# Kernel tuning notes

Measured on AMD Instinct MI355X. Metric: run time of the kernel, lower is better.

The kernel has to match this reference:

```python
import jax, jax.numpy as jnp
from jax import lax
import numpy as np

I, H, B, S = 512, 1024, 64, 512


def setup_inputs() -> dict:
    key = jax.random.key(0)
    ks = jax.random.split(key, 10)
    xav = lambda k, shape: jax.random.uniform(k, shape, jnp.float32, -1.0, 1.0) * jnp.sqrt(6.0 / (shape[0] + shape[1]))
    return {
        "x": jax.random.normal(ks[0], (B, S, I), jnp.float32),
        "wii": xav(ks[1], (I, H)), "bii": jnp.zeros((H,), jnp.float32),
        "whi": xav(ks[2], (H, H)), "bhi": jnp.zeros((H,), jnp.float32),
        "wif": xav(ks[3], (I, H)), "bif": jnp.zeros((H,), jnp.float32),
        "whf": xav(ks[4], (H, H)), "bhf": jnp.zeros((H,), jnp.float32),
        "wig": xav(ks[5], (I, H)), "big": jnp.zeros((H,), jnp.float32),
        "whg": xav(ks[6], (H, H)), "bhg": jnp.zeros((H,), jnp.float32),
        "wio": xav(ks[7], (I, H)), "bio": jnp.zeros((H,), jnp.float32),
        "who": xav(ks[8], (H, H)), "bho": jnp.zeros((H,), jnp.float32),
    }


def reference(x, wii, bii, whi, bhi, wif, bif, whf, bhf,
              wig, big, whg, bhg, wio, bio, who, bho):
    b, s, _ = x.shape
    h = wii.shape[1]
    # Fuse the four per-gate GEMMs into single (I,4H) / (H,4H) GEMMs — same math.
    Wx = jnp.concatenate([wii, wif, wig, wio], axis=1)   # (I, 4H)
    Wh = jnp.concatenate([whi, whf, whg, who], axis=1)   # (H, 4H)
    bb = jnp.concatenate([bii + bhi, bif + bhf, big + bhg, bio + bho])  # (4H,)
    xs = jnp.swapaxes(x, 0, 1)                            # (S, B, I)
    x_proj = jnp.einsum('sbi,ik->sbk', xs, Wx) + bb       # (S, B, 4H)

    def step(carry, xp):
        h_t, c_t = carry
        gates = xp + h_t @ Wh                             # (B, 4H)
        i_t, f_t, g_t, o_t = jnp.split(gates, 4, axis=-1)
        i_t = jax.nn.sigmoid(i_t)
        f_t = jax.nn.sigmoid(f_t)
        g_t = jnp.tanh(g_t)
        o_t = jax.nn.sigmoid(o_t)
        c_t = f_t * c_t + i_t * g_t
        h_t = o_t * jnp.tanh(c_t)
        return (h_t, c_t), None

    h0 = jnp.zeros((b, h), x.dtype)
    c0 = jnp.zeros((b, h), x.dtype)
    (h_T, c_T), _ = lax.scan(step, (h0, c0), x_proj)
    return (h_T, c_T)
```

## Files before the change

### kernel.cpp

```cpp
#include <hip/hip_runtime.h>
#include <hip/hip_bf16.h>
#include <stdint.h>

typedef __bf16 bf16_t;
typedef bf16_t bf16x8 __attribute__((ext_vector_type(8)));
typedef float  f32x4  __attribute__((ext_vector_type(4)));
typedef float  f32x16 __attribute__((ext_vector_type(16)));

#define I_DIM 512
#define H_DIM 1024
#define B_DIM 64
#define S_DIM 512
#define G4    4096
#define CHUNK 32
#define NCHUNK (S_DIM / CHUNK)

#define O_WXT   0x0000000ULL
#define O_WHTF  0x0400000ULL
#define O_BIAS  0x0C00000ULL
#define O_CST   0x0C10000ULL
#define O_HBUF  0x0D00000ULL
#define O_XP    0x1200000ULL

__device__ __forceinline__ float sigm(float x)      { return 1.f / (1.f + __expf(-x)); }
__device__ __forceinline__ float tanh_fast(float x) { return 1.f - 2.f / (__expf(2.f * x) + 1.f); }


__global__ void k_pack_wx(const float* __restrict__ w0, const float* __restrict__ w1,
                          const float* __restrict__ w2, const float* __restrict__ w3,
                          bf16_t* __restrict__ wxt) {
    int tid = blockIdx.x * 256 + threadIdx.x;
    int k = tid >> 12;
    int p = tid & 4095;
    int q = p >> 5, g = (p >> 3) & 3, jj = p & 7;
    int j = q * 8 + jj;
    const float* src = (g == 0) ? w0 : (g == 1) ? w1 : (g == 2) ? w2 : w3;
    wxt[(size_t)p * I_DIM + k] = (bf16_t)src[k * H_DIM + j];
}

__global__ void k_pack_whf(const float* __restrict__ w0, const float* __restrict__ w1,
                           const float* __restrict__ w2, const float* __restrict__ w3,
                           bf16_t* __restrict__ whtf) {
    int idx = blockIdx.x * 256 + threadIdx.x;
    int e    = idx & 7;
    int lane = (idx >> 3) & 63;
    int ks   = (idx >> 9) & 63;
    int q    = idx >> 15;
    int k = ks * 16 + (lane >> 5) * 8 + e;
    int c = lane & 31;
    int g = c >> 3, jj = c & 7;
    int j = q * 8 + jj;
    const float* src = (g == 0) ? w0 : (g == 1) ? w1 : (g == 2) ? w2 : w3;
    whtf[idx] = (bf16_t)src[k * H_DIM + j];
}

__global__ void k_pack_bias(const float* bi0, const float* bh0, const float* bi1, const float* bh1,
                            const float* bi2, const float* bh2, const float* bi3, const float* bh3,
                            float* __restrict__ bias) {
    int p = blockIdx.x * 256 + threadIdx.x;
    int q = p >> 5, g = (p >> 3) & 3, jj = p & 7;
    int j = q * 8 + jj;
    const float* a = (g == 0) ? bi0 : (g == 1) ? bi1 : (g == 2) ? bi2 : bi3;
    const float* b = (g == 0) ? bh0 : (g == 1) ? bh1 : (g == 2) ? bh2 : bh3;
    bias[p] = a[j] + b[j];
}

__global__ __launch_bounds__(256, 2) void k_xproj(
    const float* __restrict__ x, const bf16_t* __restrict__ wxt,
    const float* __restrict__ bias, bf16_t* __restrict__ xp, int r_base)
{
    __shared__ __align__(16) bf16_t Al[8 * 64 * 8];
    __shared__ __align__(16) bf16_t Bl[8 * 64 * 8];
    const int tid = threadIdx.x;
    const int n0 = blockIdx.x * 128;
    const int r0 = r_base + blockIdx.y * 128;
    const int wv = tid >> 6;
    const int lane = tid & 63;
    const int mq = wv >> 1, nq = wv & 1;
    f32x4 acc[4][4] = {};

    for (int kk = 0; kk < I_DIM; kk += 32) {
        __syncthreads();
        #pragma unroll
        for (int sidx = 0; sidx < 2; ++sidx) {
            int s = tid + sidx * 256;
            int mt = s >> 6, l = s & 63;
            int m = l & 15, kb = (l >> 4) * 8;
            int r = r0 + mt * 16 + m;
            int b = r & 63, si = r >> 6;
            const float* gp = x + ((size_t)(b * S_DIM + si)) * I_DIM + kk + kb;
            float4 v0 = *(const float4*)gp;
            float4 v1 = *(const float4*)(gp + 4);
            bf16x8 a;
            a[0] = (bf16_t)v0.x; a[1] = (bf16_t)v0.y; a[2] = (bf16_t)v0.z; a[3] = (bf16_t)v0.w;
            a[4] = (bf16_t)v1.x; a[5] = (bf16_t)v1.y; a[6] = (bf16_t)v1.z; a[7] = (bf16_t)v1.w;
            *(bf16x8*)&Al[s * 8] = a;
            bf16x8 bv = *(const bf16x8*)(wxt + (size_t)(n0 + mt * 16 + m) * I_DIM + kk + kb);
            *(bf16x8*)&Bl[s * 8] = bv;
        }
        __syncthreads();
        bf16x8 af[4], bfr[4];
        #pragma unroll
        for (int mt = 0; mt < 4; ++mt) af[mt]  = *(bf16x8*)&Al[((mq * 4 + mt) * 64 + lane) * 8];
        #pragma unroll
        for (int nt = 0; nt < 4; ++nt) bfr[nt] = *(bf16x8*)&Bl[((nq * 4 + nt) * 64 + lane) * 8];
        #pragma unroll
        for (int mt = 0; mt < 4; ++mt)
            #pragma unroll
            for (int nt = 0; nt < 4; ++nt)
                acc[mt][nt] = __builtin_amdgcn_mfma_f32_16x16x32_bf16(af[mt], bfr[nt], acc[mt][nt], 0, 0, 0);
    }
    const int l15 = lane & 15, quad = lane >> 4;
    #pragma unroll
    for (int nt = 0; nt < 4; ++nt) {
        int col = n0 + nq * 64 + nt * 16 + l15;
        float bv = bias[col];
        #pragma unroll
        for (int mt = 0; mt < 4; ++mt)
            #pragma unroll
            for (int r = 0; r < 4; ++r) {
                int row = r0 - r_base + mq * 64 + mt * 16 + quad * 4 + r;
                xp[(size_t)row * G4 + col] = (bf16_t)(acc[mt][nt][r] + bv);
            }
    }
}

__global__ __launch_bounds__(256, 1) void k_step(
    const bf16_t* __restrict__ whtf, const bf16_t* __restrict__ xp_t,
    const bf16_t* __restrict__ h_t, bf16_t* __restrict__ h_n,
    float* __restrict__ cstbuf, float* __restrict__ out, int write_out)
{
    __shared__ float Pl[4][16][64];
    __shared__ __align__(16) bf16_t Hlds[256];
    const int tid  = threadIdx.x;
    const int w    = tid >> 6;
    const int lane = tid & 63;
    const int bid  = blockIdx.x;
    const int q    = bid & 127;
    const int bh   = bid >> 7;

    const int col  = lane & 31;
    const int ksel = lane >> 5;
    const int gt   = (lane >> 3) & 3;
    const int jj   = lane & 7;

    int rrow[4];
    #pragma unroll
    for (int e = 0; e < 4; ++e) rrow[e] = e + 8 * w + 4 * ksel;

    bf16_t xpr[4];
    #pragma unroll
    for (int e = 0; e < 4; ++e)
        xpr[e] = xp_t[(size_t)(bh * 32 + rrow[e]) * G4 + q * 32 + col];
    float cst[4];
    if (gt == 0) {
        #pragma unroll
        for (int e = 0; e < 4; ++e)
            cst[e] = cstbuf[(bh * 32 + rrow[e]) * H_DIM + q * 8 + jj];
    }

    const bf16_t* ab = h_t  + (bh << 15) + (w << 13) + (lane << 3);
    const bf16_t* bb = whtf + ((size_t)q << 15) + (w << 13) + (lane << 3);

    bf16x8 ar[16], br[16];
    #pragma unroll
    for (int i = 0; i < 16; ++i) {
        ar[i] = *(const bf16x8*)(ab + i * 512);
        br[i] = *(const bf16x8*)(bb + i * 512);
    }
    f32x16 acc0 = {}, acc1 = {}, acc2 = {}, acc3 = {};
    #pragma unroll
    for (int i = 0; i < 16; i += 4) {
        acc0 = __builtin_amdgcn_mfma_f32_32x32x16_bf16(ar[i + 0], br[i + 0], acc0, 0, 0, 0);
        acc1 = __builtin_amdgcn_mfma_f32_32x32x16_bf16(ar[i + 1], br[i + 1], acc1, 0, 0, 0);
        acc2 = __builtin_amdgcn_mfma_f32_32x32x16_bf16(ar[i + 2], br[i + 2], acc2, 0, 0, 0);
        acc3 = __builtin_amdgcn_mfma_f32_32x32x16_bf16(ar[i + 3], br[i + 3], acc3, 0, 0, 0);
    }
    f32x16 accs = acc0 + acc1 + acc2 + acc3;

    #pragma unroll
    for (int e = 0; e < 16; ++e) Pl[w][e][lane] = accs[e];
    __syncthreads();

    #pragma unroll
    for (int e = 0; e < 4; ++e) {
        int eg = w * 4 + e;
        float pre = Pl[0][eg][lane] + Pl[1][eg][lane] + Pl[2][eg][lane] + Pl[3][eg][lane];
        pre += (float)xpr[e];
        float a = (gt == 2) ? tanh_fast(pre) : sigm(pre);

        float fv = __shfl_xor(a, 8, 64);
        float gv = __shfl_xor(a, 16, 64);
        float ov = __shfl_xor(a, 24, 64);
        if (gt == 0) {
            float cn = fv * cst[e] + a * gv;
            float hv = ov * tanh_fast(cn);
            Hlds[rrow[e] * 8 + jj] = (bf16_t)hv;
            cstbuf[(bh * 32 + rrow[e]) * H_DIM + q * 8 + jj] = cn;
            if (write_out) {
                int rowg = bh * 32 + rrow[e];
                int j = q * 8 + jj;
                out[rowg * H_DIM + j] = hv;
                out[65536 + rowg * H_DIM + j] = cn;
            }
        }
    }
    __syncthreads();

    if (w == 0) {
        uint64_t v = *(const uint64_t*)&Hlds[lane * 4];
        ((uint64_t*)h_n)[(bh << 13) + (q << 6) + lane] = v;
    }
}

extern "C" void kernel_launch(void* const* d_in, const int* in_sizes, int n_in,
                              void* d_out, int out_size, void* d_ws, size_t ws_size,
                              hipStream_t stream) {
    const float* x   = (const float*)d_in[0];
    const float* wii = (const float*)d_in[1];
    const float* bii = (const float*)d_in[2];
    const float* whi = (const float*)d_in[3];
    const float* bhi = (const float*)d_in[4];
    const float* wif = (const float*)d_in[5];
    const float* bif = (const float*)d_in[6];
    const float* whf = (const float*)d_in[7];
    const float* bhf = (const float*)d_in[8];
    const float* wig = (const float*)d_in[9];
    const float* big = (const float*)d_in[10];
    const float* whg = (const float*)d_in[11];
    const float* bhg = (const float*)d_in[12];
    const float* wio = (const float*)d_in[13];
    const float* bio = (const float*)d_in[14];
    const float* who = (const float*)d_in[15];
    const float* bho = (const float*)d_in[16];

    char* ws = (char*)d_ws;
    bf16_t*  wxt   = (bf16_t*)(ws + O_WXT);
    bf16_t*  whtf  = (bf16_t*)(ws + O_WHTF);
    float*   bias  = (float*)(ws + O_BIAS);
    float*   cstb  = (float*)(ws + O_CST);
    bf16_t*  hbuf  = (bf16_t*)(ws + O_HBUF);
    bf16_t*  xp    = (bf16_t*)(ws + O_XP);

    hipMemsetAsync(hbuf, 0, 128 * 1024, stream);
    hipMemsetAsync(cstb, 0, 256 * 1024, stream);

    k_pack_wx<<<8192, 256, 0, stream>>>(wii, wif, wig, wio, wxt);
    k_pack_whf<<<16384, 256, 0, stream>>>(whi, whf, whg, who, whtf);
    k_pack_bias<<<16, 256, 0, stream>>>(bii, bhi, bif, bhf, big, bhg, bio, bho, bias);

    float* out = (float*)d_out;
    for (int c = 0; c < NCHUNK; ++c) {
        k_xproj<<<dim3(32, CHUNK * 64 / 128), 256, 0, stream>>>(x, wxt, bias, xp, c * CHUNK * 64);
        for (int tl = 0; tl < CHUNK; ++tl) {
            int t = c * CHUNK + tl;
            k_step<<<256, 256, 0, stream>>>(
                whtf, xp + (size_t)tl * 64 * G4,
                hbuf + (size_t)(t & 1) * 65536,
                hbuf + (size_t)((t + 1) & 1) * 65536,
                cstb, out, (t == S_DIM - 1) ? 1 : 0);
        }
    }
}
```

Measured before the change: 3.462 ms.

## Make LSTM step kernel persistent per chunk with hierarchical grid barrier

Replaces the 32 per-timestep k_step launches in each chunk with one cooperative persistent kernel. The kernel loops over the chunk's timesteps and synchronizes all 256 blocks through a two-level atomic counter barrier in workspace. Each block loads its Wh slice into registers once and keeps the cell state in registers, writing it back only at chunk end. This removes launch overhead and repeated weight reloads. In exchange it relies on all blocks being co-resident, relaxed atomics for visibility of h, and spin-waiting.

New measurement: 3.344 ms. 1.04x faster.

```diff
diff --git a/kernel.cpp b/kernel.cpp
--- a/kernel.cpp
+++ b/kernel.cpp
@@ -20,6 +20,7 @@
 #define O_BIAS  0x0C00000ULL
 #define O_CST   0x0C10000ULL
 #define O_HBUF  0x0D00000ULL
+#define O_BAR   0x0D40000ULL
 #define O_XP    0x1200000ULL
 
 __device__ __forceinline__ float sigm(float x)      { return 1.f / (1.f + __expf(-x)); }
@@ -125,10 +126,11 @@
     }
 }
 
-__global__ __launch_bounds__(256, 1) void k_step(
-    const bf16_t* __restrict__ whtf, const bf16_t* __restrict__ xp_t,
-    const bf16_t* __restrict__ h_t, bf16_t* __restrict__ h_n,
-    float* __restrict__ cstbuf, float* __restrict__ out, int write_out)
+__global__ __launch_bounds__(256, 1) void k_steps(
+    const bf16_t* __restrict__ whtf, const bf16_t* __restrict__ xp_c,
+    bf16_t* __restrict__ hbuf, float* __restrict__ cstbuf,
+    float* __restrict__ out, uint32_t* __restrict__ bar,
+    int t_base, int ep_base, int write_out_last)
 {
     __shared__ float Pl[4][16][64];
     __shared__ __align__(16) bf16_t Hlds[256];
@@ -148,68 +150,110 @@
     #pragma unroll
     for (int e = 0; e < 4; ++e) rrow[e] = e + 8 * w + 4 * ksel;
 
-    bf16_t xpr[4];
+    const bf16_t* bb = whtf + ((size_t)q << 15) + (w << 13) + (lane << 3);
+    bf16x8 bfr[16];
     #pragma unroll
-    for (int e = 0; e < 4; ++e)
-        xpr[e] = xp_t[(size_t)(bh * 32 + rrow[e]) * G4 + q * 32 + col];
-    float cst[4];
+    for (int i = 0; i < 16; ++i) bfr[i] = *(const bf16x8*)(bb + i * 512);
+
+    float cst[4] = {0.f, 0.f, 0.f, 0.f};
     if (gt == 0) {
         #pragma unroll
         for (int e = 0; e < 4; ++e)
             cst[e] = cstbuf[(bh * 32 + rrow[e]) * H_DIM + q * 8 + jj];
     }
 
-    const bf16_t* ab = h_t  + (bh << 15) + (w << 13) + (lane << 3);
-    const bf16_t* bb = whtf + ((size_t)q << 15) + (w << 13) + (lane << 3);
-
-    bf16x8 ar[16], br[16];
-    #pragma unroll
-    for (int i = 0; i < 16; ++i) {
-        ar[i] = *(const bf16x8*)(ab + i * 512);
-        br[i] = *(const bf16x8*)(bb + i * 512);
-    }
-    f32x16 acc0 = {}, acc1 = {}, acc2 = {}, acc3 = {};
-    #pragma unroll
-    for (int i = 0; i < 16; i += 4) {
-        acc0 = __builtin_amdgcn_mfma_f32_32x32x16_bf16(ar[i + 0], br[i + 0], acc0, 0, 0, 0);
-        acc1 = __builtin_amdgcn_mfma_f32_32x32x16_bf16(ar[i + 1], br[i + 1], acc1, 0, 0, 0);
-        acc2 = __builtin_amdgcn_mfma_f32_32x32x16_bf16(ar[i + 2], br[i + 2], acc2, 0, 0, 0);
-        acc3 = __builtin_amdgcn_mfma_f32_32x32x16_bf16(ar[i + 3], br[i + 3], acc3, 0, 0, 0);
-    }
-    f32x16 accs = acc0 + acc1 + acc2 + acc3;
-
-    #pragma unroll
-    for (int e = 0; e < 16; ++e) Pl[w][e][lane] = accs[e];
-    __syncthreads();
-
-    #pragma unroll
-    for (int e = 0; e < 4; ++e) {
-        int eg = w * 4 + e;
-        float pre = Pl[0][eg][lane] + Pl[1][eg][lane] + Pl[2][eg][lane] + Pl[3][eg][lane];
-        pre += (float)xpr[e];
-        float a = (gt == 2) ? tanh_fast(pre) : sigm(pre);
-
-        float fv = __shfl_xor(a, 8, 64);
-        float gv = __shfl_xor(a, 16, 64);
-        float ov = __shfl_xor(a, 24, 64);
-        if (gt == 0) {
-            float cn = fv * cst[e] + a * gv;
-            float hv = ov * tanh_fast(cn);
-            Hlds[rrow[e] * 8 + jj] = (bf16_t)hv;
-            cstbuf[(bh * 32 + rrow[e]) * H_DIM + q * 8 + jj] = cn;
-            if (write_out) {
-                int rowg = bh * 32 + rrow[e];
-                int j = q * 8 + jj;
-                out[rowg * H_DIM + j] = hv;
-                out[65536 + rowg * H_DIM + j] = cn;
+    const int abase = (bh << 15) + (w << 13) + (lane << 3);
+
+    for (int tl = 0; tl < CHUNK; ++tl) {
+        const bf16_t* xp_t = xp_c + (size_t)(tl * 64) * G4;
+        uint64_t* hsrc = (uint64_t*)(hbuf + (((t_base + tl) & 1) << 16) + abase);
+
+        uint64_t hl0[16], hl1[16];
+        #pragma unroll
+        for (int i = 0; i < 16; ++i) {
+            hl0[i] = __hip_atomic_load(hsrc + i * 128,     __ATOMIC_RELAXED, __HIP_MEMORY_SCOPE_AGENT);
+            hl1[i] = __hip_atomic_load(hsrc + i * 128 + 1, __ATOMIC_RELAXED, __HIP_MEMORY_SCOPE_AGENT);
+        }
+
+        bf16_t xpr[4];
+        #pragma unroll
+        for (int e = 0; e < 4; ++e)
+            xpr[e] = xp_t[(size_t)(bh * 32 + rrow[e]) * G4 + q * 32 + col];
+
+        struct U2 { uint64_t a, b; };
+        f32x16 acc0 = {}, acc1 = {}, acc2 = {}, acc3 = {};
+        #pragma unroll
+        for (int i = 0; i < 16; i += 4) {
+            U2 t0{hl0[i + 0], hl1[i + 0]};
+            U2 t1{hl0[i + 1], hl1[i + 1]};
+            U2 t2{hl0[i + 2], hl1[i + 2]};
+            U2 t3{hl0[i + 3], hl1[i + 3]};
+            acc0 = __builtin_amdgcn_mfma_f32_32x32x16_bf16(__builtin_bit_cast(bf16x8, t0), bfr[i + 0], acc0, 0, 0, 0);
+            acc1 = __builtin_amdgcn_mfma_f32_32x32x16_bf16(__builtin_bit_cast(bf16x8, t1), bfr[i + 1], acc1, 0, 0, 0);
+            acc2 = __builtin_amdgcn_mfma_f32_32x32x16_bf16(__builtin_bit_cast(bf16x8, t2), bfr[i + 2], acc2, 0, 0, 0);
+            acc3 = __builtin_amdgcn_mfma_f32_32x32x16_bf16(__builtin_bit_cast(bf16x8, t3), bfr[i + 3], acc3, 0, 0, 0);
+        }
+        f32x16 accs = acc0 + acc1 + acc2 + acc3;
+
+        #pragma unroll
+        for (int e = 0; e < 16; ++e) Pl[w][e][lane] = accs[e];
+        __syncthreads();
+
+        #pragma unroll
+        for (int e = 0; e < 4; ++e) {
+            int eg = w * 4 + e;
+            float pre = Pl[0][eg][lane] + Pl[1][eg][lane] + Pl[2][eg][lane] + Pl[3][eg][lane];
+            pre += (float)xpr[e];
+            float a = (gt == 2) ? tanh_fast(pre) : sigm(pre);
+
+            float fv = __shfl_xor(a, 8, 64);
+            float gv = __shfl_xor(a, 16, 64);
+            float ov = __shfl_xor(a, 24, 64);
+            if (gt == 0) {
+                float cn = fv * cst[e] + a * gv;
+                float hv = ov * tanh_fast(cn);
+                cst[e] = cn;
+                Hlds[rrow[e] * 8 + jj] = (bf16_t)hv;
+                if (write_out_last && tl == CHUNK - 1) {
+                    int rowg = bh * 32 + rrow[e];
+                    int j = q * 8 + jj;
+                    out[rowg * H_DIM + j] = hv;
+                    out[65536 + rowg * H_DIM + j] = cn;
+                }
             }
         }
-    }
-    __syncthreads();
-
-    if (w == 0) {
-        uint64_t v = *(const uint64_t*)&Hlds[lane * 4];
-        ((uint64_t*)h_n)[(bh << 13) + (q << 6) + lane] = v;
+        __syncthreads();
+
+        if (w == 0) {
+            uint64_t v = *(const uint64_t*)&Hlds[lane * 4];
+            uint64_t* hdst = (uint64_t*)(hbuf + (((t_base + tl + 1) & 1) << 16));
+            __hip_atomic_store(hdst + (bh << 13) + (q << 6) + lane, v,
+                               __ATOMIC_RELAXED, __HIP_MEMORY_SCOPE_AGENT);
+        }
+
+        if (tl < CHUNK - 1) {
+            __syncthreads();
+            if (tid == 0) {
+                uint32_t old = __hip_atomic_fetch_add(&bar[(bid & 7) * 64], 1u,
+                                                      __ATOMIC_RELAXED, __HIP_MEMORY_SCOPE_AGENT);
+                if ((old & 31u) == 31u) {
+                    uint32_t old2 = __hip_atomic_fetch_add(&bar[512], 1u,
+                                                           __ATOMIC_RELAXED, __HIP_MEMORY_SCOPE_AGENT);
+                    if ((old2 & 7u) == 7u)
+                        __hip_atomic_fetch_add(&bar[576], 1u,
+                                               __ATOMIC_RELAXED, __HIP_MEMORY_SCOPE_AGENT);
+                }
+                uint32_t target = (uint32_t)(ep_base + tl + 1);
+                while (__hip_atomic_load(&bar[576], __ATOMIC_RELAXED, __HIP_MEMORY_SCOPE_AGENT) < target) {}
+            }
+            __syncthreads();
+        }
+    }
+
+    if (gt == 0) {
+        #pragma unroll
+        for (int e = 0; e < 4; ++e)
+            cstbuf[(bh * 32 + rrow[e]) * H_DIM + q * 8 + jj] = cst[e];
     }
 }
 
@@ -235,15 +279,17 @@
     const float* bho = (const float*)d_in[16];
 
     char* ws = (char*)d_ws;
-    bf16_t*  wxt   = (bf16_t*)(ws + O_WXT);
-    bf16_t*  whtf  = (bf16_t*)(ws + O_WHTF);
-    float*   bias  = (float*)(ws + O_BIAS);
-    float*   cstb  = (float*)(ws + O_CST);
-    bf16_t*  hbuf  = (bf16_t*)(ws + O_HBUF);
-    bf16_t*  xp    = (bf16_t*)(ws + O_XP);
+    bf16_t*   wxt  = (bf16_t*)(ws + O_WXT);
+    bf16_t*   whtf = (bf16_t*)(ws + O_WHTF);
+    float*    bias = (float*)(ws + O_BIAS);
+    float*    cstb = (float*)(ws + O_CST);
+    bf16_t*   hbuf = (bf16_t*)(ws + O_HBUF);
+    uint32_t* bar  = (uint32_t*)(ws + O_BAR);
+    bf16_t*   xp   = (bf16_t*)(ws + O_XP);
 
     hipMemsetAsync(hbuf, 0, 128 * 1024, stream);
     hipMemsetAsync(cstb, 0, 256 * 1024, stream);
+    hipMemsetAsync(bar,  0, 4096, stream);
 
     k_pack_wx<<<8192, 256, 0, stream>>>(wii, wif, wig, wio, wxt);
     k_pack_whf<<<16384, 256, 0, stream>>>(whi, whf, whg, who, whtf);
@@ -252,13 +298,16 @@
     float* out = (float*)d_out;
     for (int c = 0; c < NCHUNK; ++c) {
         k_xproj<<<dim3(32, CHUNK * 64 / 128), 256, 0, stream>>>(x, wxt, bias, xp, c * CHUNK * 64);
-        for (int tl = 0; tl < CHUNK; ++tl) {
-            int t = c * CHUNK + tl;
-            k_step<<<256, 256, 0, stream>>>(
-                whtf, xp + (size_t)tl * 64 * G4,
-                hbuf + (size_t)(t & 1) * 65536,
-                hbuf + (size_t)((t + 1) & 1) * 65536,
-                cstb, out, (t == S_DIM - 1) ? 1 : 0);
-        }
-    }
-}
+        int t_base  = c * CHUNK;
+        int ep_base = c * (CHUNK - 1);
+        int wol     = (c == NCHUNK - 1) ? 1 : 0;
+        void* args[] = { (void*)&whtf, (void*)&xp, (void*)&hbuf, (void*)&cstb,
+                         (void*)&out, (void*)&bar, (void*)&t_base, (void*)&ep_base, (void*)&wol };
+        hipError_t err = hipLaunchCooperativeKernel((const void*)k_steps, dim3(256), dim3(256),
+                                                    args, 0, stream);
+        if (err != hipSuccess) {
+            k_steps<<<256, 256, 0, stream>>>(whtf, xp, hbuf, cstb, out, bar,
+                                             t_base, ep_base, wol);
+        }
+    }
+}
```
